# Kernel optimization log

Measured on AMD Instinct MI355X. Metric: run time of the kernel, lower is better.

Reference implementation:

```python
import jax, jax.numpy as jnp
import numpy as np

LN_EPS = 1e-5


def setup_inputs() -> dict:
    key = jax.random.key(0)
    ks = jax.random.split(key, 5)
    N, E, D = 50000, 600000, 128
    x = jax.random.normal(ks[0], (N, D), dtype=jnp.float32)
    edge_index = jax.random.randint(ks[1], (2, E), 0, N, dtype=jnp.int64)
    W_l = jax.random.normal(ks[2], (D, D), dtype=jnp.float32) * (1.0 / np.sqrt(D))
    b_l = jnp.zeros((D,), dtype=jnp.float32)
    W_r = jax.random.normal(ks[3], (D, D), dtype=jnp.float32) * (1.0 / np.sqrt(D))
    gamma = jnp.ones((D,), dtype=jnp.float32)
    beta = jnp.zeros((D,), dtype=jnp.float32)
    return {"x": x, "edge_index": edge_index, "W_l": W_l, "b_l": b_l,
            "W_r": W_r, "gamma": gamma, "beta": beta}


def reference(x, edge_index, W_l, b_l, W_r, gamma, beta):
    # SAGEConv (mean aggregation): out = lin_l(mean_{j in N(i)} x_j) + lin_r(x_i)
    N = x.shape[0]
    src, dst = edge_index[0], edge_index[1]
    msg = x[src]                                                # (E, D) gather
    agg = jax.ops.segment_sum(msg, dst, num_segments=N)         # (N, D) scatter-add
    cnt = jax.ops.segment_sum(jnp.ones_like(dst, dtype=x.dtype), dst, num_segments=N)
    mean = agg / jnp.maximum(cnt, 1.0)[:, None]
    h = mean @ W_l.T + b_l + x @ W_r.T                          # (N, D)
    # LayerNorm over feature dim
    mu = jnp.mean(h, axis=-1, keepdims=True)
    var = jnp.mean(jnp.square(h - mu), axis=-1, keepdims=True)
    h = (h - mu) * jax.lax.rsqrt(var + LN_EPS) * gamma + beta
    # ReLU; Dropout is identity in eval mode
    return jax.nn.relu(h)
```

## Files before the change

kernel.cpp:

```cpp
#include <hip/hip_runtime.h>
#include <stdint.h>

#define DIM 128
#define LN_EPS 1e-5f
#define BROWS 32
#define BCAP 768
#define LELLS 56
#define LOVF 64
#define ATS 264
#define PINIT ((int)0xAAAAAAAA)

typedef __attribute__((ext_vector_type(8))) short bf16x8;
typedef __attribute__((ext_vector_type(4))) float f32x4;

static __device__ __forceinline__ uint16_t f2bf(float f) {
    uint32_t u = __float_as_uint(f);
    return (uint16_t)((u + 0x7fffu + ((u >> 16) & 1u)) >> 16);
}
static __device__ __forceinline__ float bf_lo(uint32_t w) {
    return __uint_as_float(w << 16);
}
static __device__ __forceinline__ float bf_hi(uint32_t w) {
    return __uint_as_float(w & 0xffff0000u);
}

__global__ __launch_bounds__(256) void prep_kernel(
    const int* __restrict__ ei,
    const float* __restrict__ Wl,
    const float* __restrict__ Wr,
    const float* __restrict__ x,
    int* __restrict__ bcnt, int* __restrict__ novf, int* __restrict__ ovf,
    uint32_t* __restrict__ bedge,
    uint16_t* __restrict__ wc, uint16_t* __restrict__ x16,
    int E, int N)
{
    int tid = blockIdx.x * blockDim.x + threadIdx.x;
    int nth = gridDim.x * blockDim.x;

    int npair = (E + 1) >> 1;
    for (int pe = tid; pe < npair; pe += nth) {
        int e0 = 2 * pe;
        int n = (e0 + 1 < E) ? 2 : ((e0 < E) ? 1 : 0);
        int ss[2], dd[2];
        if (n == 2) {
            int2 s2 = *(const int2*)(ei + e0);
            int2 d2 = *(const int2*)(ei + E + e0);
            ss[0] = s2.x; ss[1] = s2.y; dd[0] = d2.x; dd[1] = d2.y;
        } else if (n == 1) {
            ss[0] = ei[e0]; dd[0] = ei[E + e0];
        }
        for (int k = 0; k < n; ++k) {
            int src = ss[k], dst = dd[k];
            int bkt = dst >> 5;
            int r = atomicAdd(bcnt + (size_t)bkt * 16, 1) - PINIT;
            if (r >= 0 && r < BCAP) {
                bedge[(size_t)bkt * BCAP + r] =
                    ((uint32_t)(dst & 31) << 27) | (uint32_t)src;
            } else if (r >= BCAP) {
                int q = atomicAdd(novf, 1) - PINIT;
                if (q >= 0 && q < E) { ovf[2 * q] = dst; ovf[2 * q + 1] = src; }
            }
        }
    }

    int nxp = (N * DIM) >> 1;
    for (int i = tid; i < nxp; i += nth) {
        float2 v = *(const float2*)(x + 2 * i);
        uint32_t u = ((uint32_t)f2bf(v.y) << 16) | (uint32_t)f2bf(v.x);
        ((uint32_t*)x16)[i] = u;
    }

    for (int i = tid; i < DIM * 256; i += nth) {
        int d = i >> 8, k = i & 255;
        float v = (k < DIM) ? Wl[d * DIM + k] : Wr[d * DIM + (k - DIM)];
        wc[i] = f2bf(v);
    }
}

__global__ __launch_bounds__(256, 4) void fused_kernel(
    const uint16_t* __restrict__ x16,
    const int* __restrict__ bcnt,
    const uint32_t* __restrict__ bedge,
    const int* __restrict__ novf,
    const int* __restrict__ ovf,
    const uint16_t* __restrict__ wc,
    const float* __restrict__ bl,
    const float* __restrict__ gma,
    const float* __restrict__ bta,
    float* __restrict__ out,
    int N, int E)
{
    __shared__ int ell_s[BROWS][LELLS];
    __shared__ int cnt_s[BROWS];
    __shared__ int lovf_s[LOVF];
    __shared__ int nlovf_s;
    __shared__ uint16_t atile[2][16 * ATS];
    __shared__ float pln[2][16][2][2];

    const int t    = threadIdx.x;
    const int lane = t & 63;
    const int w    = t >> 6;
    const int p    = w >> 1;
    const int h    = w & 1;
    const int blk_row0  = blockIdx.x * BROWS;
    const int tile_row0 = blk_row0 + p * 16;
    const int grow0     = tile_row0 + h * 8;
    const int lb        = p * 16 + h * 8;

    if (t < BROWS) cnt_s[t] = 0;
    if (t == BROWS) nlovf_s = 0;
    __syncthreads();

    {
        int bc = bcnt[(size_t)blockIdx.x * 16] - PINIT;
        bc = (bc < 0) ? 0 : (bc > BCAP ? BCAP : bc);
        const uint32_t* bptr = bedge + (size_t)blockIdx.x * BCAP;
        for (int i = t; i < bc; i += 256) {
            uint32_t pk = bptr[i];
            int local = pk >> 27;
            int src   = pk & 0x07FFFFFF;
            int r = atomicAdd(&cnt_s[local], 1);
            if (r < LELLS) ell_s[local][r] = src;
            else {
                int q = atomicAdd(&nlovf_s, 1);
                if (q < LOVF) lovf_s[q] = (int)pk;
            }
        }
    }
    __syncthreads();

    int dgx[8], nell[8], mx = 0;
    #pragma unroll
    for (int r = 0; r < 8; ++r) {
        int d = __builtin_amdgcn_readfirstlane(cnt_s[lb + r]);
        dgx[r] = d;
        int tt = d < LELLS ? d : LELLS;
        nell[r] = tt;
        mx = (tt > mx) ? tt : mx;
    }

    int sidx[8];
    #pragma unroll
    for (int r = 0; r < 8; ++r)
        sidx[r] = (lane < nell[r]) ? ell_s[lb + r][lane] : 0;

    float m0[8], m1[8];
    #pragma unroll
    for (int r = 0; r < 8; ++r) { m0[r] = 0.0f; m1[r] = 0.0f; }

    for (int j = 0; j < mx; ++j) {
        #pragma unroll
        for (int r = 0; r < 8; ++r) {
            float pr = (j < nell[r]) ? 1.0f : 0.0f;
            int s = __builtin_amdgcn_readlane(sidx[r], j);
            uint32_t u = *(const uint32_t*)(x16 + (size_t)s * DIM + 2 * lane);
            m0[r] = fmaf(pr, bf_lo(u), m0[r]);
            m1[r] = fmaf(pr, bf_hi(u), m1[r]);
        }
    }

    {
        int nl = __builtin_amdgcn_readfirstlane(nlovf_s);
        nl = (nl < 0) ? 0 : (nl > LOVF ? LOVF : nl);
        for (int i = 0; i < nl; ++i) {
            uint32_t pk = (uint32_t)lovf_s[i];
            int local = pk >> 27;
            if (local >= lb && local < lb + 8) {
                int srco = pk & 0x07FFFFFF;
                uint32_t u = *(const uint32_t*)(x16 + (size_t)srco * DIM + 2 * lane);
                float v0 = bf_lo(u), v1 = bf_hi(u);
                #pragma unroll
                for (int r = 0; r < 8; ++r) {
                    float pr = (local == lb + r) ? 1.0f : 0.0f;
                    m0[r] = fmaf(pr, v0, m0[r]);
                    m1[r] = fmaf(pr, v1, m1[r]);
                }
            }
        }
    }

    {
        int no = __builtin_amdgcn_readfirstlane(novf[0]) - PINIT;
        no = (no < 0) ? 0 : (no > E ? E : no);
        for (int i = 0; i < no; ++i) {
            int dsto = __builtin_amdgcn_readfirstlane(ovf[2 * i]);
            int srco = __builtin_amdgcn_readfirstlane(ovf[2 * i + 1]);
            if (dsto >= grow0 && dsto < grow0 + 8) {
                uint32_t u = *(const uint32_t*)(x16 + (size_t)srco * DIM + 2 * lane);
                float v0 = bf_lo(u), v1 = bf_hi(u);
                #pragma unroll
                for (int r = 0; r < 8; ++r) {
                    bool hit = (dsto == grow0 + r);
                    float pr = hit ? 1.0f : 0.0f;
                    m0[r] = fmaf(pr, v0, m0[r]);
                    m1[r] = fmaf(pr, v1, m1[r]);
                    dgx[r] += hit ? 1 : 0;
                }
            }
        }
    }

    {
        uint16_t* at = atile[p];
        #pragma unroll
        for (int r = 0; r < 8; ++r) {
            int row = grow0 + r;
            int rr = (row < N) ? row : 0;
            float rc = (dgx[r] > 0) ? (1.0f / (float)dgx[r]) : 0.0f;
            int lr = h * 8 + r;
            ushort2 mu2;
            mu2.x = f2bf(m0[r] * rc);
            mu2.y = f2bf(m1[r] * rc);
            *(ushort2*)&at[lr * ATS + 2 * lane] = mu2;
            uint32_t xv = *(const uint32_t*)(x16 + (size_t)rr * DIM + 2 * lane);
            *(uint32_t*)&at[lr * ATS + 128 + 2 * lane] = xv;
        }
    }
    __syncthreads();

    const int nsub = lane & 15;
    const int quad = lane >> 4;
    const uint16_t* at = atile[p];

    f32x4 acc[4];
    #pragma unroll
    for (int tt = 0; tt < 4; ++tt) {
        float b = bl[(h * 4 + tt) * 16 + nsub];
        acc[tt] = (f32x4){b, b, b, b};
    }

    #pragma unroll
    for (int c = 0; c < 8; ++c) {
        bf16x8 af = *(const bf16x8*)&at[nsub * ATS + c * 32 + quad * 8];
        #pragma unroll
        for (int tt = 0; tt < 4; ++tt) {
            int tg = h * 4 + tt;
            bf16x8 bfr = *(const bf16x8*)&wc[(size_t)(tg * 16 + nsub) * 256 + c * 32 + quad * 8];
            acc[tt] = __builtin_amdgcn_mfma_f32_16x16x32_bf16(af, bfr, acc[tt], 0, 0, 0);
        }
    }

    #pragma unroll
    for (int i = 0; i < 4; ++i) {
        float s = 0.0f, q = 0.0f;
        #pragma unroll
        for (int tt = 0; tt < 4; ++tt) {
            float v = acc[tt][i];
            s += v;
            q += v * v;
        }
        #pragma unroll
        for (int off = 1; off < 16; off <<= 1) {
            s += __shfl_xor(s, off, 64);
            q += __shfl_xor(q, off, 64);
        }
        if (nsub == 0) {
            pln[p][quad * 4 + i][h][0] = s;
            pln[p][quad * 4 + i][h][1] = q;
        }
    }
    __syncthreads();

    #pragma unroll
    for (int i = 0; i < 4; ++i) {
        int lrow = quad * 4 + i;
        float s = pln[p][lrow][0][0] + pln[p][lrow][1][0];
        float q = pln[p][lrow][0][1] + pln[p][lrow][1][1];
        float mu = s * (1.0f / 128.0f);
        float var = q * (1.0f / 128.0f) - mu * mu;
        float rs = rsqrtf(fmaxf(var, 0.0f) + LN_EPS);
        int grow = tile_row0 + lrow;
        if (grow < N) {
            float* op = out + (size_t)grow * DIM;
            #pragma unroll
            for (int tt = 0; tt < 4; ++tt) {
                int f = (h * 4 + tt) * 16 + nsub;
                float o = fmaxf((acc[tt][i] - mu) * rs * gma[f] + bta[f], 0.0f);
                op[f] = o;
            }
        }
    }
}

extern "C" void kernel_launch(void* const* d_in, const int* in_sizes, int n_in,
                              void* d_out, int out_size, void* d_ws, size_t ws_size,
                              hipStream_t stream) {
    const float* x  = (const float*)d_in[0];
    const int* ei   = (const int*)d_in[1];
    const float* Wl = (const float*)d_in[2];
    const float* bl = (const float*)d_in[3];
    const float* Wr = (const float*)d_in[4];
    const float* ga = (const float*)d_in[5];
    const float* be = (const float*)d_in[6];
    float* out = (float*)d_out;

    int N = in_sizes[0] / DIM;
    int E = in_sizes[1] / 2;
    int nbkt = (N + BROWS - 1) / BROWS;

    int* bcnt      = (int*)d_ws;
    int* novf      = bcnt + (size_t)nbkt * 16;
    uint16_t* wc   = (uint16_t*)(novf + 16);
    uint16_t* x16  = wc + DIM * 256;
    uint32_t* bedge = (uint32_t*)(x16 + (size_t)N * DIM);
    int* ovf       = (int*)(bedge + (size_t)nbkt * BCAP);

    prep_kernel<<<(E / 2 + 255) / 256, 256, 0, stream>>>(
        ei, Wl, Wr, x, bcnt, novf, ovf, bedge, wc, x16, E, N);

    fused_kernel<<<nbkt, 256, 0, stream>>>(
        x16, bcnt, bedge, novf, ovf, wc, bl, ga, be, out, N, E);
}
```

Baseline: 188.2 us.

## Replace global-atomic edge bucketing with per-block shared-memory histogram binning

Edge binning switches from global atomic counters per destination bucket to a fixed grid of 128 blocks. Each block counts its slice of edges in a shared-memory histogram, then writes them into per-(bucket, block) slots of capacity 16, with a small global overflow list. The fused kernel now gathers each bucket's edges by having 128 threads walk their slot lists instead of reading one contiguous bucket array. This removes contended global atomics and the padded counters. In exchange it reads edge_index twice, uses a larger sparse edge buffer, and runs the x/W bf16 conversion on only 128 blocks, which may leave much of the GPU idle.

```diff
diff --git a/kernel.cpp b/kernel.cpp
--- a/kernel.cpp
+++ b/kernel.cpp
@@ -4,9 +4,12 @@
 #define DIM 128
 #define LN_EPS 1e-5f
 #define BROWS 32
-#define BCAP 768
+#define BINB 128
+#define SCAP 16
+#define NBKT_MAX 1600
 #define LELLS 56
 #define LOVF 64
+#define OVFCAP 4096
 #define ATS 264
 #define PINIT ((int)0xAAAAAAAA)
 
@@ -24,62 +27,69 @@
     return __uint_as_float(w & 0xffff0000u);
 }
 
-__global__ __launch_bounds__(256) void prep_kernel(
+__global__ __launch_bounds__(256) void bin_kernel(
     const int* __restrict__ ei,
+    const float* __restrict__ x,
     const float* __restrict__ Wl,
     const float* __restrict__ Wr,
-    const float* __restrict__ x,
-    int* __restrict__ bcnt, int* __restrict__ novf, int* __restrict__ ovf,
-    uint32_t* __restrict__ bedge,
-    uint16_t* __restrict__ wc, uint16_t* __restrict__ x16,
-    int E, int N)
+    int* __restrict__ cnt, uint32_t* __restrict__ bedge,
+    int* __restrict__ novf, int* __restrict__ ovf,
+    uint16_t* __restrict__ x16, uint16_t* __restrict__ wc,
+    int E, int N, int nbkt)
 {
-    int tid = blockIdx.x * blockDim.x + threadIdx.x;
-    int nth = gridDim.x * blockDim.x;
-
-    int npair = (E + 1) >> 1;
-    for (int pe = tid; pe < npair; pe += nth) {
-        int e0 = 2 * pe;
-        int n = (e0 + 1 < E) ? 2 : ((e0 < E) ? 1 : 0);
-        int ss[2], dd[2];
-        if (n == 2) {
-            int2 s2 = *(const int2*)(ei + e0);
-            int2 d2 = *(const int2*)(ei + E + e0);
-            ss[0] = s2.x; ss[1] = s2.y; dd[0] = d2.x; dd[1] = d2.y;
-        } else if (n == 1) {
-            ss[0] = ei[e0]; dd[0] = ei[E + e0];
-        }
-        for (int k = 0; k < n; ++k) {
-            int src = ss[k], dst = dd[k];
-            int bkt = dst >> 5;
-            int r = atomicAdd(bcnt + (size_t)bkt * 16, 1) - PINIT;
-            if (r >= 0 && r < BCAP) {
-                bedge[(size_t)bkt * BCAP + r] =
-                    ((uint32_t)(dst & 31) << 27) | (uint32_t)src;
-            } else if (r >= BCAP) {
-                int q = atomicAdd(novf, 1) - PINIT;
-                if (q >= 0 && q < E) { ovf[2 * q] = dst; ovf[2 * q + 1] = src; }
-            }
-        }
-    }
-
-    int nxp = (N * DIM) >> 1;
-    for (int i = tid; i < nxp; i += nth) {
-        float2 v = *(const float2*)(x + 2 * i);
-        uint32_t u = ((uint32_t)f2bf(v.y) << 16) | (uint32_t)f2bf(v.x);
-        ((uint32_t*)x16)[i] = u;
-    }
-
-    for (int i = tid; i < DIM * 256; i += nth) {
-        int d = i >> 8, k = i & 255;
-        float v = (k < DIM) ? Wl[d * DIM + k] : Wr[d * DIM + (k - DIM)];
-        wc[i] = f2bf(v);
+    __shared__ int hist[NBKT_MAX];
+    const int t = threadIdx.x, b = blockIdx.x;
+
+    for (int i = t; i < nbkt; i += 256) hist[i] = 0;
+    __syncthreads();
+
+    const int chunk = (E + BINB - 1) / BINB;
+    const int e0 = b * chunk;
+    const int e1 = (e0 + chunk < E) ? e0 + chunk : E;
+
+    for (int e = e0 + t; e < e1; e += 256)
+        atomicAdd(&hist[ei[E + e] >> 5], 1);
+    __syncthreads();
+
+    for (int i = t; i < nbkt; i += 256) {
+        cnt[(size_t)i * BINB + b] = hist[i];
+        hist[i] = 0;
+    }
+    __syncthreads();
+
+    for (int e = e0 + t; e < e1; e += 256) {
+        int src = ei[e];
+        int dst = ei[E + e];
+        int bkt = dst >> 5;
+        int r = atomicAdd(&hist[bkt], 1);
+        if (r < SCAP) {
+            bedge[((size_t)bkt * BINB + b) * SCAP + r] =
+                ((uint32_t)(dst & 31) << 27) | (uint32_t)src;
+        } else {
+            int q = atomicAdd(novf, 1) - PINIT;
+            if (q >= 0 && q < OVFCAP) { ovf[2 * q] = dst; ovf[2 * q + 1] = src; }
+        }
+    }
+
+    {
+        int tid = b * 256 + t, nth = BINB * 256;
+        int nxp = (N * DIM) >> 1;
+        for (int i = tid; i < nxp; i += nth) {
+            float2 v = *(const float2*)(x + 2 * i);
+            uint32_t u = ((uint32_t)f2bf(v.y) << 16) | (uint32_t)f2bf(v.x);
+            ((uint32_t*)x16)[i] = u;
+        }
+        for (int i = tid; i < DIM * 256; i += nth) {
+            int d = i >> 8, k = i & 255;
+            float v = (k < DIM) ? Wl[d * DIM + k] : Wr[d * DIM + (k - DIM)];
+            wc[i] = f2bf(v);
+        }
     }
 }
 
 __global__ __launch_bounds__(256, 4) void fused_kernel(
     const uint16_t* __restrict__ x16,
-    const int* __restrict__ bcnt,
+    const int* __restrict__ cnt,
     const uint32_t* __restrict__ bedge,
     const int* __restrict__ novf,
     const int* __restrict__ ovf,
@@ -102,8 +112,7 @@
     const int w    = t >> 6;
     const int p    = w >> 1;
     const int h    = w & 1;
-    const int blk_row0  = blockIdx.x * BROWS;
-    const int tile_row0 = blk_row0 + p * 16;
+    const int tile_row0 = blockIdx.x * BROWS + p * 16;
     const int grow0     = tile_row0 + h * 8;
     const int lb        = p * 16 + h * 8;
 
@@ -111,16 +120,15 @@
     if (t == BROWS) nlovf_s = 0;
     __syncthreads();
 
-    {
-        int bc = bcnt[(size_t)blockIdx.x * 16] - PINIT;
-        bc = (bc < 0) ? 0 : (bc > BCAP ? BCAP : bc);
-        const uint32_t* bptr = bedge + (size_t)blockIdx.x * BCAP;
-        for (int i = t; i < bc; i += 256) {
-            uint32_t pk = bptr[i];
+    if (t < BINB) {
+        int c = cnt[(size_t)blockIdx.x * BINB + t];
+        c = (c < SCAP) ? c : SCAP;
+        const uint32_t* sp = bedge + ((size_t)blockIdx.x * BINB + t) * SCAP;
+        for (int r = 0; r < c; ++r) {
+            uint32_t pk = sp[r];
             int local = pk >> 27;
-            int src   = pk & 0x07FFFFFF;
-            int r = atomicAdd(&cnt_s[local], 1);
-            if (r < LELLS) ell_s[local][r] = src;
+            int rr = atomicAdd(&cnt_s[local], 1);
+            if (rr < LELLS) ell_s[local][rr] = (int)(pk & 0x07FFFFFF);
             else {
                 int q = atomicAdd(&nlovf_s, 1);
                 if (q < LOVF) lovf_s[q] = (int)pk;
@@ -166,7 +174,7 @@
             uint32_t pk = (uint32_t)lovf_s[i];
             int local = pk >> 27;
             if (local >= lb && local < lb + 8) {
-                int srco = pk & 0x07FFFFFF;
+                int srco = (int)(pk & 0x07FFFFFF);
                 uint32_t u = *(const uint32_t*)(x16 + (size_t)srco * DIM + 2 * lane);
                 float v0 = bf_lo(u), v1 = bf_hi(u);
                 #pragma unroll
@@ -181,7 +189,7 @@
 
     {
         int no = __builtin_amdgcn_readfirstlane(novf[0]) - PINIT;
-        no = (no < 0) ? 0 : (no > E ? E : no);
+        no = (no < 0) ? 0 : (no > OVFCAP ? OVFCAP : no);
         for (int i = 0; i < no; ++i) {
             int dsto = __builtin_amdgcn_readfirstlane(ovf[2 * i]);
             int srco = __builtin_amdgcn_readfirstlane(ovf[2 * i + 1]);
@@ -298,16 +306,16 @@
     int E = in_sizes[1] / 2;
     int nbkt = (N + BROWS - 1) / BROWS;
 
-    int* bcnt      = (int*)d_ws;
-    int* novf      = bcnt + (size_t)nbkt * 16;
-    uint16_t* wc   = (uint16_t*)(novf + 16);
-    uint16_t* x16  = wc + DIM * 256;
+    int* cnt        = (int*)d_ws;
+    int* novf       = cnt + (size_t)nbkt * BINB;
+    uint16_t* wc    = (uint16_t*)(novf + 16);
+    uint16_t* x16   = wc + DIM * 256;
     uint32_t* bedge = (uint32_t*)(x16 + (size_t)N * DIM);
-    int* ovf       = (int*)(bedge + (size_t)nbkt * BCAP);
-
-    prep_kernel<<<(E / 2 + 255) / 256, 256, 0, stream>>>(
-        ei, Wl, Wr, x, bcnt, novf, ovf, bedge, wc, x16, E, N);
+    int* ovf        = (int*)(bedge + (size_t)nbkt * BINB * SCAP);
+
+    bin_kernel<<<BINB, 256, 0, stream>>>(
+        ei, x, Wl, Wr, cnt, bedge, novf, ovf, x16, wc, E, N, nbkt);
 
     fused_kernel<<<nbkt, 256, 0, stream>>>(
-        x16, bcnt, bedge, novf, ovf, wc, bl, ga, be, out, N, E);
-}
+        x16, cnt, bedge, novf, ovf, wc, bl, ga, be, out, N, E);
+}
```

New measurement: 187.2 us. No clear change (-0.5%).
